# Optimization experiments

Hardware: AMD Instinct MI355X
Metric: run time of the kernel (lower is better)

The kernel has to match this reference:

```python
import jax, jax.numpy as jnp
import numpy as np

CH_IN, CH_Y = 32, 16
B, H, W = 16, 256, 256


def setup_inputs() -> dict:
    key = jax.random.key(0)
    ks = jax.random.split(key, 10)
    scale_in = 1.0 / np.sqrt(CH_IN)
    scale_y = 1.0 / np.sqrt(CH_Y)
    return {
        "c": jax.random.normal(ks[0], (B, CH_IN, H, W), dtype=jnp.float32),
        "p": jax.random.normal(ks[1], (B, CH_IN, H, W), dtype=jnp.float32),
        "Wq": jax.random.uniform(ks[2], (CH_Y, CH_IN), jnp.float32, -scale_in, scale_in),
        "bq": jax.random.uniform(ks[3], (CH_Y,), jnp.float32, -scale_in, scale_in),
        "Wk": jax.random.uniform(ks[4], (CH_Y, CH_IN), jnp.float32, -scale_in, scale_in),
        "bk": jax.random.uniform(ks[5], (CH_Y,), jnp.float32, -scale_in, scale_in),
        "Wv": jax.random.uniform(ks[6], (CH_Y, CH_IN), jnp.float32, -scale_in, scale_in),
        "bv": jax.random.uniform(ks[7], (CH_Y,), jnp.float32, -scale_in, scale_in),
        "Wy": jax.random.uniform(ks[8], (CH_IN, CH_Y), jnp.float32, -scale_y, scale_y),
        "by": jax.random.uniform(ks[9], (CH_IN,), jnp.float32, -scale_y, scale_y),
    }


def _conv1x1(x, w, b):
    # x: [B,C,H,W], w: [O,C], b: [O] -> [B,O,H,W]
    return jnp.einsum("bchw,oc->bohw", x, w) + b[None, :, None, None]


def reference(c, p, Wq, bq, Wk, bk, Wv, bv, Wy, by):
    q = _conv1x1(c, Wq, bq)
    k = _conv1x1(p, Wk, bk)
    v = _conv1x1(p, Wv, bv)
    y = jax.nn.softmax(q * k, axis=-1)  # softmax over width
    y = y * v
    y = _conv1x1(y, Wy, by)
    return jnp.concatenate((y, c), axis=1)  # [B, 2*CH_IN, H, W]
```

## Files before the change

kernel.cpp:

```cpp
#include <hip/hip_runtime.h>

#define CH_IN 32
#define CH_Y  16
#define Bn    16
#define Hn    256
#define Wn    256
#define HW    (Hn * Wn)

typedef float f32x4 __attribute__((ext_vector_type(4)));

template<int ctrl, int rm, int bm>
__device__ __forceinline__ float dpp0(float x) {
    union { float f; int i; } u, r;
    u.f = x;
    r.i = __builtin_amdgcn_update_dpp(0, u.i, ctrl, rm, bm, false);
    return r.f;
}

__device__ __forceinline__ float wave_sum64(float x) {
    x += dpp0<0x111, 0xf, 0xf>(x);
    x += dpp0<0x112, 0xf, 0xf>(x);
    x += dpp0<0x114, 0xf, 0xf>(x);
    x += dpp0<0x118, 0xf, 0xf>(x);
    x += dpp0<0x142, 0xa, 0xf>(x);
    x += dpp0<0x143, 0xc, 0xf>(x);
    union { float f; int i; } u, r;
    u.f = x;
    r.i = __builtin_amdgcn_readlane(u.i, 63);
    return r.f;
}

__global__ __launch_bounds__(64, 3)
void CrossModalAttn_kernel(
    const float* __restrict__ cin, const float* __restrict__ pin,
    const float* __restrict__ Wq,  const float* __restrict__ bq,
    const float* __restrict__ Wk,  const float* __restrict__ bk,
    const float* __restrict__ Wv,  const float* __restrict__ bv,
    const float* __restrict__ Wy,  const float* __restrict__ by,
    float* __restrict__ out)
{
    const int bh   = blockIdx.x;
    const int b    = bh >> 8;
    const int h    = bh & 255;
    const int lane = threadIdx.x;
    const int w0   = lane << 2;

    const size_t rowoff = (size_t)h * Wn + w0;
    const float* pbase = pin + (size_t)b * CH_IN * HW + rowoff;
    const float* cbase = cin + (size_t)b * CH_IN * HW + rowoff;
    float*       obase = out + (size_t)b * (2 * CH_IN) * HW + rowoff;

    f32x4 qq[CH_Y];
    #pragma unroll
    for (int o = 0; o < CH_Y; ++o) {
        float t = bq[o];
        qq[o] = (f32x4){t, t, t, t};
    }
    #pragma unroll 4
    for (int cc = 0; cc < CH_IN; ++cc) {
        f32x4 x = __builtin_nontemporal_load(
            (const f32x4*)(cbase + (size_t)cc * HW));
        __builtin_nontemporal_store(
            x, (f32x4*)(obase + (size_t)(CH_IN + cc) * HW));
        #pragma unroll
        for (int o = 0; o < CH_Y; ++o) {
            float wgt = Wq[o * CH_IN + cc];
            qq[o].x = fmaf(wgt, x.x, qq[o].x);
            qq[o].y = fmaf(wgt, x.y, qq[o].y);
            qq[o].z = fmaf(wgt, x.z, qq[o].z);
            qq[o].w = fmaf(wgt, x.w, qq[o].w);
        }
    }

    f32x4 kk[CH_Y];
    #pragma unroll
    for (int o = 0; o < CH_Y; ++o) {
        float t = bk[o];
        kk[o] = (f32x4){t, t, t, t};
    }
    #pragma unroll 4
    for (int cc = 0; cc < CH_IN; ++cc) {
        f32x4 x = *(const f32x4*)(pbase + (size_t)cc * HW);
        #pragma unroll
        for (int o = 0; o < CH_Y; ++o) {
            float wgt = Wk[o * CH_IN + cc];
            kk[o].x = fmaf(wgt, x.x, kk[o].x);
            kk[o].y = fmaf(wgt, x.y, kk[o].y);
            kk[o].z = fmaf(wgt, x.z, kk[o].z);
            kk[o].w = fmaf(wgt, x.w, kk[o].w);
        }
    }

    f32x4 ee[CH_Y];
    #pragma unroll
    for (int o = 0; o < CH_Y; ++o) {
        f32x4 e;
        e.x = __expf(qq[o].x * kk[o].x);
        e.y = __expf(qq[o].y * kk[o].y);
        e.z = __expf(qq[o].z * kk[o].z);
        e.w = __expf(qq[o].w * kk[o].w);
        float s   = (e.x + e.y) + (e.z + e.w);
        float tot = wave_sum64(s);
        float r   = __builtin_amdgcn_rcpf(tot);
        e.x *= r; e.y *= r; e.z *= r; e.w *= r;
        ee[o] = e;
    }

    f32x4 vv[CH_Y];
    #pragma unroll
    for (int o = 0; o < CH_Y; ++o) {
        float t = bv[o];
        vv[o] = (f32x4){t, t, t, t};
    }
    #pragma unroll 4
    for (int cc = 0; cc < CH_IN; ++cc) {
        f32x4 x = *(const f32x4*)(pbase + (size_t)cc * HW);
        #pragma unroll
        for (int o = 0; o < CH_Y; ++o) {
            float wgt = Wv[o * CH_IN + cc];
            vv[o].x = fmaf(wgt, x.x, vv[o].x);
            vv[o].y = fmaf(wgt, x.y, vv[o].y);
            vv[o].z = fmaf(wgt, x.z, vv[o].z);
            vv[o].w = fmaf(wgt, x.w, vv[o].w);
        }
    }

    #pragma unroll
    for (int o = 0; o < CH_Y; ++o) {
        ee[o].x *= vv[o].x;
        ee[o].y *= vv[o].y;
        ee[o].z *= vv[o].z;
        ee[o].w *= vv[o].w;
    }

    #pragma unroll 4
    for (int co = 0; co < CH_IN; ++co) {
        float t = by[co];
        f32x4 acc = (f32x4){t, t, t, t};
        #pragma unroll
        for (int o = 0; o < CH_Y; ++o) {
            float wgt = Wy[co * CH_Y + o];
            acc.x = fmaf(wgt, ee[o].x, acc.x);
            acc.y = fmaf(wgt, ee[o].y, acc.y);
            acc.z = fmaf(wgt, ee[o].z, acc.z);
            acc.w = fmaf(wgt, ee[o].w, acc.w);
        }
        __builtin_nontemporal_store(
            acc, (f32x4*)(obase + (size_t)co * HW));
    }
}

extern "C" void kernel_launch(void* const* d_in, const int* in_sizes, int n_in,
                              void* d_out, int out_size, void* d_ws, size_t ws_size,
                              hipStream_t stream) {
    const float* c  = (const float*)d_in[0];
    const float* p  = (const float*)d_in[1];
    const float* Wq = (const float*)d_in[2];
    const float* bq = (const float*)d_in[3];
    const float* Wk = (const float*)d_in[4];
    const float* bk = (const float*)d_in[5];
    const float* Wv = (const float*)d_in[6];
    const float* bv = (const float*)d_in[7];
    const float* Wy = (const float*)d_in[8];
    const float* by = (const float*)d_in[9];
    float* out = (float*)d_out;

    dim3 grid(Bn * Hn);
    dim3 block(64);
    hipLaunchKernelGGL(CrossModalAttn_kernel, grid, block, 0, stream,
                       c, p, Wq, bq, Wk, bk, Wv, bv, Wy, by, out);
}
```

Measured before the change: 477.6 us.

## Cut register pressure by computing K and V in groups of four channels

Computes K and V projections in groups of four output channels, reusing the q register array in place for the exponentials and deferring the softmax normalisation into the V multiply. This frees the full 16-entry K, E and V register arrays so the launch bound can rise from three to four waves per SIMD. In exchange the p input is re-read four times per projection (eight passes over p instead of two), which relies on cache hits. The c load is also switched from nontemporal to a normal load.

```diff
diff --git a/kernel.cpp b/kernel.cpp
--- a/kernel.cpp
+++ b/kernel.cpp
@@ -30,7 +30,7 @@
     return r.f;
 }
 
-__global__ __launch_bounds__(64, 3)
+__global__ __launch_bounds__(64, 4)
 void CrossModalAttn_kernel(
     const float* __restrict__ cin, const float* __restrict__ pin,
     const float* __restrict__ Wq,  const float* __restrict__ bq,
@@ -50,87 +50,91 @@
     const float* cbase = cin + (size_t)b * CH_IN * HW + rowoff;
     float*       obase = out + (size_t)b * (2 * CH_IN) * HW + rowoff;
 
-    f32x4 qq[CH_Y];
+    f32x4 qe[CH_Y];
     #pragma unroll
     for (int o = 0; o < CH_Y; ++o) {
         float t = bq[o];
-        qq[o] = (f32x4){t, t, t, t};
+        qe[o] = (f32x4){t, t, t, t};
     }
     #pragma unroll 4
     for (int cc = 0; cc < CH_IN; ++cc) {
-        f32x4 x = __builtin_nontemporal_load(
-            (const f32x4*)(cbase + (size_t)cc * HW));
+        f32x4 x = *(const f32x4*)(cbase + (size_t)cc * HW);
         __builtin_nontemporal_store(
             x, (f32x4*)(obase + (size_t)(CH_IN + cc) * HW));
         #pragma unroll
         for (int o = 0; o < CH_Y; ++o) {
             float wgt = Wq[o * CH_IN + cc];
-            qq[o].x = fmaf(wgt, x.x, qq[o].x);
-            qq[o].y = fmaf(wgt, x.y, qq[o].y);
-            qq[o].z = fmaf(wgt, x.z, qq[o].z);
-            qq[o].w = fmaf(wgt, x.w, qq[o].w);
+            qe[o].x = fmaf(wgt, x.x, qe[o].x);
+            qe[o].y = fmaf(wgt, x.y, qe[o].y);
+            qe[o].z = fmaf(wgt, x.z, qe[o].z);
+            qe[o].w = fmaf(wgt, x.w, qe[o].w);
         }
     }
 
-    f32x4 kk[CH_Y];
+    float rr[CH_Y];
     #pragma unroll
-    for (int o = 0; o < CH_Y; ++o) {
-        float t = bk[o];
-        kk[o] = (f32x4){t, t, t, t};
-    }
-    #pragma unroll 4
-    for (int cc = 0; cc < CH_IN; ++cc) {
-        f32x4 x = *(const f32x4*)(pbase + (size_t)cc * HW);
+    for (int og = 0; og < CH_Y / 4; ++og) {
+        f32x4 kk4[4];
         #pragma unroll
-        for (int o = 0; o < CH_Y; ++o) {
-            float wgt = Wk[o * CH_IN + cc];
-            kk[o].x = fmaf(wgt, x.x, kk[o].x);
-            kk[o].y = fmaf(wgt, x.y, kk[o].y);
-            kk[o].z = fmaf(wgt, x.z, kk[o].z);
-            kk[o].w = fmaf(wgt, x.w, kk[o].w);
+        for (int j = 0; j < 4; ++j) {
+            float t = bk[og * 4 + j];
+            kk4[j] = (f32x4){t, t, t, t};
         }
-    }
-
-    f32x4 ee[CH_Y];
-    #pragma unroll
-    for (int o = 0; o < CH_Y; ++o) {
-        f32x4 e;
-        e.x = __expf(qq[o].x * kk[o].x);
-        e.y = __expf(qq[o].y * kk[o].y);
-        e.z = __expf(qq[o].z * kk[o].z);
-        e.w = __expf(qq[o].w * kk[o].w);
-        float s   = (e.x + e.y) + (e.z + e.w);
-        float tot = wave_sum64(s);
-        float r   = __builtin_amdgcn_rcpf(tot);
-        e.x *= r; e.y *= r; e.z *= r; e.w *= r;
-        ee[o] = e;
-    }
-
-    f32x4 vv[CH_Y];
-    #pragma unroll
-    for (int o = 0; o < CH_Y; ++o) {
-        float t = bv[o];
-        vv[o] = (f32x4){t, t, t, t};
-    }
-    #pragma unroll 4
-    for (int cc = 0; cc < CH_IN; ++cc) {
-        f32x4 x = *(const f32x4*)(pbase + (size_t)cc * HW);
+        #pragma unroll 4
+        for (int cc = 0; cc < CH_IN; ++cc) {
+            f32x4 x = *(const f32x4*)(pbase + (size_t)cc * HW);
+            #pragma unroll
+            for (int j = 0; j < 4; ++j) {
+                float wgt = Wk[(og * 4 + j) * CH_IN + cc];
+                kk4[j].x = fmaf(wgt, x.x, kk4[j].x);
+                kk4[j].y = fmaf(wgt, x.y, kk4[j].y);
+                kk4[j].z = fmaf(wgt, x.z, kk4[j].z);
+                kk4[j].w = fmaf(wgt, x.w, kk4[j].w);
+            }
+        }
         #pragma unroll
-        for (int o = 0; o < CH_Y; ++o) {
-            float wgt = Wv[o * CH_IN + cc];
-            vv[o].x = fmaf(wgt, x.x, vv[o].x);
-            vv[o].y = fmaf(wgt, x.y, vv[o].y);
-            vv[o].z = fmaf(wgt, x.z, vv[o].z);
-            vv[o].w = fmaf(wgt, x.w, vv[o].w);
+        for (int j = 0; j < 4; ++j) {
+            const int o = og * 4 + j;
+            f32x4 e;
+            e.x = __expf(qe[o].x * kk4[j].x);
+            e.y = __expf(qe[o].y * kk4[j].y);
+            e.z = __expf(qe[o].z * kk4[j].z);
+            e.w = __expf(qe[o].w * kk4[j].w);
+            float s = (e.x + e.y) + (e.z + e.w);
+            rr[o] = __builtin_amdgcn_rcpf(wave_sum64(s));
+            qe[o] = e;
         }
     }
 
     #pragma unroll
-    for (int o = 0; o < CH_Y; ++o) {
-        ee[o].x *= vv[o].x;
-        ee[o].y *= vv[o].y;
-        ee[o].z *= vv[o].z;
-        ee[o].w *= vv[o].w;
+    for (int og = 0; og < CH_Y / 4; ++og) {
+        f32x4 vv4[4];
+        #pragma unroll
+        for (int j = 0; j < 4; ++j) {
+            float t = bv[og * 4 + j];
+            vv4[j] = (f32x4){t, t, t, t};
+        }
+        #pragma unroll 4
+        for (int cc = 0; cc < CH_IN; ++cc) {
+            f32x4 x = *(const f32x4*)(pbase + (size_t)cc * HW);
+            #pragma unroll
+            for (int j = 0; j < 4; ++j) {
+                float wgt = Wv[(og * 4 + j) * CH_IN + cc];
+                vv4[j].x = fmaf(wgt, x.x, vv4[j].x);
+                vv4[j].y = fmaf(wgt, x.y, vv4[j].y);
+                vv4[j].z = fmaf(wgt, x.z, vv4[j].z);
+                vv4[j].w = fmaf(wgt, x.w, vv4[j].w);
+            }
+        }
+        #pragma unroll
+        for (int j = 0; j < 4; ++j) {
+            const int o = og * 4 + j;
+            float r = rr[o];
+            qe[o].x *= r * vv4[j].x;
+            qe[o].y *= r * vv4[j].y;
+            qe[o].z *= r * vv4[j].z;
+            qe[o].w *= r * vv4[j].w;
+        }
     }
 
     #pragma unroll 4
@@ -140,10 +144,10 @@
         #pragma unroll
         for (int o = 0; o < CH_Y; ++o) {
             float wgt = Wy[co * CH_Y + o];
-            acc.x = fmaf(wgt, ee[o].x, acc.x);
-            acc.y = fmaf(wgt, ee[o].y, acc.y);
-            acc.z = fmaf(wgt, ee[o].z, acc.z);
-            acc.w = fmaf(wgt, ee[o].w, acc.w);
+            acc.x = fmaf(wgt, qe[o].x, acc.x);
+            acc.y = fmaf(wgt, qe[o].y, acc.y);
+            acc.z = fmaf(wgt, qe[o].z, acc.z);
+            acc.w = fmaf(wgt, qe[o].w, acc.w);
         }
         __builtin_nontemporal_store(
             acc, (f32x4*)(obase + (size_t)co * HW));
```

Result: slower. 574.9 us (+20.4%).
